# Performance work log

Measured on AMD Instinct MI355X. Metric: run time of the kernel, lower is better.

The kernel has to match this reference:

```python
import jax, jax.numpy as jnp
import numpy as np

N_VERTS = 778
N_JOINTS_CHAIN = 16  # wrist + 15 articulated joints
N_JOINTS_ALL = 21
PARENTS = np.array([0, 0, 1, 2, 0, 4, 5, 0, 7, 8, 0, 10, 11, 0, 13, 14])


def rodrigues(r):
    """Axis-angle [N,3] -> rotation matrices [N,3,3] (matches torch quat2mat path)."""
    angle = jnp.linalg.norm(r + 1e-8, axis=1, keepdims=True)  # [N,1]
    axis = r / angle
    c = jnp.cos(angle)[..., None]  # [N,1,1]
    s = jnp.sin(angle)[..., None]
    x, y, z = axis[:, 0], axis[:, 1], axis[:, 2]
    zero = jnp.zeros_like(x)
    K = jnp.stack([zero, -z, y,
                   z, zero, -x,
                   -y, x, zero], axis=1).reshape(-1, 3, 3)
    eye = jnp.eye(3, dtype=r.dtype)
    return eye + s * K + (1.0 - c) * jnp.matmul(K, K)


def make_A(R, t):
    """R [B,3,3], t [B,3] -> homogeneous [B,4,4]."""
    B = R.shape[0]
    top = jnp.concatenate([R, t[:, :, None]], axis=2)  # [B,3,4]
    bottom = jnp.broadcast_to(jnp.array([[[0., 0., 0., 1.]]], dtype=R.dtype), (B, 1, 4))
    return jnp.concatenate([top, bottom], axis=1)


def setup_inputs() -> dict:
    key = jax.random.key(0)
    ks = jax.random.split(key, 10)
    B = 8192
    w = jax.random.uniform(ks[9], (N_VERTS, 16), dtype=jnp.float32)
    w = w / jnp.sum(w, axis=1, keepdims=True)  # LBS weights rows sum to 1
    Jr = jax.random.uniform(ks[6], (N_VERTS, N_JOINTS_ALL), dtype=jnp.float32)
    Jr = Jr / jnp.sum(Jr, axis=0, keepdims=True)
    return {
        "beta": jax.random.normal(ks[0], (B, 10), dtype=jnp.float32) * 0.5,
        "theta": jax.random.normal(ks[1], (B, 10), dtype=jnp.float32) * 0.5,
        "wrist_euler": jax.random.normal(ks[2], (B, 3), dtype=jnp.float32) * 0.3,
        "v_template": jax.random.normal(ks[3], (N_VERTS, 3), dtype=jnp.float32) * 0.05,
        "shapedirs": jax.random.normal(ks[4], (10, N_VERTS * 3), dtype=jnp.float32) * 0.01,
        "posedirs": jax.random.normal(ks[5], (135, N_VERTS * 3), dtype=jnp.float32) * 0.01,
        "J_regressor": Jr,
        "hands_comp": jax.random.normal(ks[7], (10, 45), dtype=jnp.float32) * 0.5,
        "hands_mean": jax.random.normal(ks[8], (45,), dtype=jnp.float32) * 0.1,
        "weights": w,
    }


def reference(beta, theta, wrist_euler, v_template, shapedirs, posedirs,
              J_regressor, hands_comp, hands_mean, weights):
    B = beta.shape[0]
    # shape blendshapes
    v_shaped = jnp.matmul(beta, shapedirs).reshape(B, N_VERTS, 3) + v_template
    # joints from shaped template: [B,21,3]
    J = jnp.einsum('bvc,vj->bjc', v_shaped, J_regressor)
    # pca pose -> per-joint axis-angle -> rotation matrices
    euler_pose = jnp.matmul(theta, hands_comp) + hands_mean          # [B,45]
    Rs = rodrigues(euler_pose.reshape(-1, 3)).reshape(B, 15, 3, 3)
    global_rot = rodrigues(wrist_euler.reshape(-1, 3)).reshape(B, 1, 3, 3)
    # pose blendshapes: (Rs - I) flattened
    pose_feature = (Rs - jnp.eye(3, dtype=Rs.dtype)).reshape(B, 135)
    v_posed = v_shaped + jnp.matmul(pose_feature, posedirs).reshape(B, N_VERTS, 3)
    # kinematic chain (16 joints, fixed small loop)
    Rs_all = jnp.concatenate([global_rot, Rs], axis=1)  # [B,16,3,3]
    Jc = J[:, :N_JOINTS_CHAIN, :]
    results = [make_A(Rs_all[:, 0], Jc[:, 0])]
    for i in range(1, N_JOINTS_CHAIN):
        p = int(PARENTS[i])
        A_local = make_A(Rs_all[:, i], Jc[:, i] - Jc[:, p])
        results.append(jnp.matmul(results[p], A_local))
    G = jnp.stack(results, axis=1)  # [B,16,4,4]
    # subtract rest-pose joint locations: A = G - G @ [J;0] in last column
    Jh = jnp.concatenate([Jc, jnp.zeros((B, N_JOINTS_CHAIN, 1), Jc.dtype)], axis=2)
    GJ = jnp.einsum('bjpq,bjq->bjp', G, Jh)  # [B,16,4]
    A = G - jnp.concatenate([jnp.zeros((B, N_JOINTS_CHAIN, 4, 3), G.dtype), GJ[..., None]], axis=3)
    # linear blend skinning
    T = jnp.einsum('vj,bjpq->bvpq', weights, A)  # [B,778,4,4]
    v_posed_h = jnp.concatenate([v_posed, jnp.ones((B, N_VERTS, 1), v_posed.dtype)], axis=2)
    verts = jnp.einsum('bvpq,bvq->bvp', T, v_posed_h)[:, :, :3]
    joints = jnp.einsum('bvc,vj->bjc', verts, J_regressor)  # [B,21,3]
    return joints
```

## Files before the change

kernel.cpp:

```cpp
#include <hip/hip_runtime.h>
#include <math.h>

#define NV 778
#define KROW 2334
#define KTOT 146
#define NCOL 1008
#define NPART 16
#define DTLD 160

__global__ __launch_bounds__(64) void kA_pre(const float* __restrict__ shapedirs,
                                             const float* __restrict__ posedirs,
                                             const float* __restrict__ v_template,
                                             const float* __restrict__ Jreg,
                                             const float* __restrict__ wgt,
                                             float* __restrict__ SJ, float* __restrict__ J0,
                                             float* __restrict__ Q,  float* __restrict__ W2,
                                             float* __restrict__ DT, int w2_blocks)
{
    const int bid = blockIdx.x;
    const int t = threadIdx.x;
    if (bid < 48) {
        const int j = bid / 3, c = bid % 3;
        float acc[11];
#pragma unroll
        for (int k = 0; k < 11; ++k) acc[k] = 0.f;
        for (int v = t; v < NV; v += 64) {
            const float jr = Jreg[v*21 + j];
            acc[10] += v_template[v*3 + c] * jr;
#pragma unroll
            for (int k = 0; k < 10; ++k)
                acc[k] += shapedirs[(size_t)k*KROW + v*3 + c] * jr;
        }
#pragma unroll
        for (int k = 0; k < 11; ++k) {
            float s = acc[k];
#pragma unroll
            for (int off = 32; off >= 1; off >>= 1) s += __shfl_down(s, off, 64);
            acc[k] = s;
        }
        if (t == 0) {
#pragma unroll
            for (int k = 0; k < 10; ++k) SJ[k*48 + j*3 + c] = acc[k];
            J0[j*3 + c] = acc[10];
        }
    } else if (bid < 384) {
        const int m = bid - 48, j = m >> 4, jj = m & 15;
        float s = 0.f;
        for (int v = t; v < NV; v += 64)
            s += Jreg[v*21 + j] * wgt[v*16 + jj];
#pragma unroll
        for (int off = 32; off >= 1; off >>= 1) s += __shfl_down(s, off, 64);
        if (t == 0) Q[m] = s;
    } else if (bid < 384 + w2_blocks) {
        const int gi = (bid - 384)*64 + t;
        if (gi < NV*336) {
            const int v = gi / 336, m = gi % 336;
            const int j = m >> 4, jj = m & 15;
            W2[gi] = Jreg[v*21 + j] * wgt[v*16 + jj];
        }
    } else {
        const int v = bid - 384 - w2_blocks;
#pragma unroll
        for (int kk = 0; kk < 3; ++kk) {
            const int k = t + kk*64;
            if (k < KTOT) {
                const float* drow = (k < 10)  ? shapedirs + (size_t)k*KROW
                                  : (k < 145) ? posedirs + (size_t)(k-10)*KROW
                                              : v_template;
                DT[((size_t)0*NV + v)*DTLD + k] = drow[3*v + 0];
                DT[((size_t)1*NV + v)*DTLD + k] = drow[3*v + 1];
                DT[((size_t)2*NV + v)*DTLD + k] = drow[3*v + 2];
            }
        }
    }
}

__global__ __launch_bounds__(192) void k_pre2(const float* __restrict__ DT,
                                              const float* __restrict__ W2,
                                              float* __restrict__ PKpart)
{
    const int bid = blockIdx.x;
    const int j = bid % 21;
    const int c = (bid / 21) % 3;
    const int s = bid / 63;
    const int k = threadIdx.x;
    if (k >= KTOT) return;
    float acc[16];
#pragma unroll
    for (int q = 0; q < 16; ++q) acc[q] = 0.f;
    const int v0 = s*49, v1 = min(NV, v0 + 49);
    const float* dt = DT + ((size_t)c*NV)*DTLD + k;
    for (int v = v0; v < v1; ++v) {
        const float d = dt[(size_t)v*DTLD];
        const float4* wq = (const float4*)(W2 + (size_t)v*336 + j*16);
        const float4 w0 = wq[0], w1 = wq[1], w2 = wq[2], w3 = wq[3];
        acc[0]  += d*w0.x; acc[1]  += d*w0.y; acc[2]  += d*w0.z; acc[3]  += d*w0.w;
        acc[4]  += d*w1.x; acc[5]  += d*w1.y; acc[6]  += d*w1.z; acc[7]  += d*w1.w;
        acc[8]  += d*w2.x; acc[9]  += d*w2.y; acc[10] += d*w2.z; acc[11] += d*w2.w;
        acc[12] += d*w3.x; acc[13] += d*w3.y; acc[14] += d*w3.z; acc[15] += d*w3.w;
    }
    float* o = PKpart + ((size_t)s*KTOT + k)*NCOL + j*48 + c;
#pragma unroll
    for (int q = 0; q < 16; ++q) o[q*3] = acc[q];
}

__global__ void k_p3(const float4* __restrict__ PKpart, float4* __restrict__ PK)
{
    const int n4 = KTOT*NCOL/4;
    const int idx = blockIdx.x*256 + threadIdx.x;
    if (idx < n4) {
        float4 s = PKpart[idx];
#pragma unroll
        for (int p = 1; p < NPART; ++p) {
            const float4 v = PKpart[(size_t)p*n4 + idx];
            s.x += v.x; s.y += v.y; s.z += v.z; s.w += v.w;
        }
        PK[idx] = s;
    }
}

__global__ __launch_bounds__(256) void k2_pose(const float* __restrict__ beta,
                                               const float* __restrict__ theta,
                                               const float* __restrict__ wrist,
                                               const float* __restrict__ hc,
                                               const float* __restrict__ hm,
                                               const float* __restrict__ SJ,
                                               const float* __restrict__ J0,
                                               float* __restrict__ coefT,
                                               float* __restrict__ A_g, int B)
{
    __shared__ float Rs[16*144];
    __shared__ float cls[16*148];
    const int t = threadIdx.x;
    const int bl = t >> 4, i = t & 15;
    const int b = blockIdx.x*16 + bl;

    float r0, r1, r2;
    if (i == 0) {
        r0 = wrist[b*3+0]; r1 = wrist[b*3+1]; r2 = wrist[b*3+2];
#pragma unroll
        for (int k = 0; k < 10; ++k) cls[bl*148 + k] = beta[b*10 + k];
        cls[bl*148 + 145] = 1.0f;
    } else {
        const int col = (i-1)*3;
        float e0 = hm[col], e1 = hm[col+1], e2 = hm[col+2];
#pragma unroll
        for (int k = 0; k < 10; ++k) {
            const float th = theta[b*10 + k];
            e0 += th * hc[k*45 + col];
            e1 += th * hc[k*45 + col+1];
            e2 += th * hc[k*45 + col+2];
        }
        r0 = e0; r1 = e1; r2 = e2;
    }
    const float x_ = r0 + 1e-8f, y_ = r1 + 1e-8f, z_ = r2 + 1e-8f;
    const float angle = sqrtf(x_*x_ + y_*y_ + z_*z_);
    const float inv = 1.0f / angle;
    const float x = r0*inv, y = r1*inv, z = r2*inv;
    const float sn = sinf(angle), cs = cosf(angle);
    const float t1 = 1.0f - cs;
    float R[9];
    R[0] = 1.f - t1*(y*y + z*z);
    R[1] = -sn*z + t1*x*y;
    R[2] =  sn*y + t1*x*z;
    R[3] =  sn*z + t1*x*y;
    R[4] = 1.f - t1*(x*x + z*z);
    R[5] = -sn*x + t1*y*z;
    R[6] = -sn*y + t1*x*z;
    R[7] =  sn*x + t1*y*z;
    R[8] = 1.f - t1*(x*x + y*y);
#pragma unroll
    for (int q = 0; q < 9; ++q) Rs[bl*144 + i*9 + q] = R[q];
    if (i > 0) {
#pragma unroll
        for (int q = 0; q < 9; ++q)
            cls[bl*148 + 10 + (i-1)*9 + q] = R[q] - ((q==0||q==4||q==8) ? 1.f : 0.f);
    }
    __syncthreads();

    if (t < KTOT) {
        float tmp[16];
#pragma unroll
        for (int m = 0; m < 16; ++m) tmp[m] = cls[m*148 + t];
        float4* dst = (float4*)(coefT + (size_t)t*B + blockIdx.x*16);
        dst[0] = make_float4(tmp[0],  tmp[1],  tmp[2],  tmp[3]);
        dst[1] = make_float4(tmp[4],  tmp[5],  tmp[6],  tmp[7]);
        dst[2] = make_float4(tmp[8],  tmp[9],  tmp[10], tmp[11]);
        dst[3] = make_float4(tmp[12], tmp[13], tmp[14], tmp[15]);
    }

    if (t < 16) {
        const int b2 = blockIdx.x*16 + t;
        float bt[10];
#pragma unroll
        for (int k = 0; k < 10; ++k) bt[k] = beta[b2*10 + k];
        const float* Rb = Rs + t*144;
        float4* Ab = (float4*)(A_g + (size_t)b2*192);

        auto jointJ = [&](int j, float* o) {
            float j0 = J0[j*3+0], j1 = J0[j*3+1], j2 = J0[j*3+2];
#pragma unroll
            for (int k = 0; k < 10; ++k) {
                j0 += bt[k] * SJ[k*48 + j*3 + 0];
                j1 += bt[k] * SJ[k*48 + j*3 + 1];
                j2 += bt[k] * SJ[k*48 + j*3 + 2];
            }
            o[0] = j0; o[1] = j1; o[2] = j2;
        };

        float G0R[9], J0v[3];
#pragma unroll
        for (int q = 0; q < 9; ++q) G0R[q] = Rb[q];
        jointJ(0, J0v);
#pragma unroll
        for (int r = 0; r < 3; ++r) {
            const float at = J0v[r] - (G0R[r*3+0]*J0v[0] + G0R[r*3+1]*J0v[1] + G0R[r*3+2]*J0v[2]);
            Ab[r] = make_float4(G0R[r*3+0], G0R[r*3+1], G0R[r*3+2], at);
        }
        for (int ch = 0; ch < 5; ++ch) {
            float GpR[9], Gpt[3], Jp[3];
#pragma unroll
            for (int q = 0; q < 9; ++q) GpR[q] = G0R[q];
            Gpt[0]=J0v[0]; Gpt[1]=J0v[1]; Gpt[2]=J0v[2];
            Jp[0]=J0v[0];  Jp[1]=J0v[1];  Jp[2]=J0v[2];
            for (int s = 0; s < 3; ++s) {
                const int j = ch*3 + 1 + s;
                float Rl[9];
                const float* Rj = Rb + j*9;
#pragma unroll
                for (int q = 0; q < 9; ++q) Rl[q] = Rj[q];
                float Jc[3];
                jointJ(j, Jc);
                const float tl0 = Jc[0]-Jp[0], tl1 = Jc[1]-Jp[1], tl2 = Jc[2]-Jp[2];
                float GR[9], Gt[3];
#pragma unroll
                for (int r = 0; r < 3; ++r) {
#pragma unroll
                    for (int cc = 0; cc < 3; ++cc)
                        GR[r*3+cc] = GpR[r*3+0]*Rl[0*3+cc] + GpR[r*3+1]*Rl[1*3+cc] + GpR[r*3+2]*Rl[2*3+cc];
                    Gt[r] = GpR[r*3+0]*tl0 + GpR[r*3+1]*tl1 + GpR[r*3+2]*tl2 + Gpt[r];
                }
#pragma unroll
                for (int r = 0; r < 3; ++r) {
                    const float at = Gt[r] - (GR[r*3+0]*Jc[0] + GR[r*3+1]*Jc[1] + GR[r*3+2]*Jc[2]);
                    Ab[j*3 + r] = make_float4(GR[r*3+0], GR[r*3+1], GR[r*3+2], at);
                }
#pragma unroll
                for (int q = 0; q < 9; ++q) GpR[q] = GR[q];
                Gpt[0]=Gt[0]; Gpt[1]=Gt[1]; Gpt[2]=Gt[2];
                Jp[0]=Jc[0];  Jp[1]=Jc[1];  Jp[2]=Jc[2];
            }
        }
    }
}

__global__ __launch_bounds__(256) void k3_gemm(const float* __restrict__ coefT,
                                               const float* __restrict__ PK,
                                               const float* __restrict__ A_g,
                                               const float* __restrict__ Q,
                                               float* __restrict__ out, int B)
{
    __shared__ float Pex[48*256];
    const int t  = threadIdx.x;
    const int b0 = blockIdx.x * 256;
    const int j  = blockIdx.y;
    const int ci = __builtin_amdgcn_readfirstlane(t >> 6);
    const int bi = t & 63;

    float acc[12][4];
#pragma unroll
    for (int m = 0; m < 12; ++m)
#pragma unroll
        for (int e = 0; e < 4; ++e) acc[m][e] = 0.f;

    const float* pkbase = PK + j*48 + 4*ci;
    const float* cbase  = coefT + b0 + 4*bi;

#pragma unroll 2
    for (int k = 0; k < KTOT; ++k) {
        const float4 c4 = *(const float4*)(cbase + (size_t)k*B);
        const float* pr = pkbase + (size_t)k*NCOL;
        const float4 p0 = *(const float4*)(pr);
        const float4 p1 = *(const float4*)(pr + 16);
        const float4 p2 = *(const float4*)(pr + 32);
        const float pv[12] = {p0.x,p0.y,p0.z,p0.w, p1.x,p1.y,p1.z,p1.w, p2.x,p2.y,p2.z,p2.w};
        const float cv[4]  = {c4.x,c4.y,c4.z,c4.w};
#pragma unroll
        for (int m = 0; m < 12; ++m)
#pragma unroll
            for (int e = 0; e < 4; ++e)
                acc[m][e] += pv[m] * cv[e];
    }

#pragma unroll
    for (int m = 0; m < 12; ++m) {
        const int col = 16*(m >> 2) + 4*ci + (m & 3);
        *(float4*)(&Pex[col*256 + 4*bi]) =
            make_float4(acc[m][0], acc[m][1], acc[m][2], acc[m][3]);
    }
    __syncthreads();

    {
        const int b = b0 + t;
        const float4* Ab = ((const float4*)A_g) + (size_t)b*48;
        const float* Pr = Pex + t;
        float jx = 0.f, jy = 0.f, jz = 0.f;
#pragma unroll
        for (int jj = 0; jj < 16; ++jj) {
            const float qv = Q[j*16 + jj];
            const float4 a0 = Ab[jj*3+0];
            const float4 a1 = Ab[jj*3+1];
            const float4 a2 = Ab[jj*3+2];
            const float px = Pr[(jj*3+0)*256];
            const float py = Pr[(jj*3+1)*256];
            const float pz = Pr[(jj*3+2)*256];
            jx += a0.x*px + a0.y*py + a0.z*pz + a0.w*qv;
            jy += a1.x*px + a1.y*py + a1.z*pz + a1.w*qv;
            jz += a2.x*px + a2.y*py + a2.z*pz + a2.w*qv;
        }
        float* op = out + (size_t)b*63 + j*3;
        op[0] = jx; op[1] = jy; op[2] = jz;
    }
}

extern "C" void kernel_launch(void* const* d_in, const int* in_sizes, int n_in,
                              void* d_out, int out_size, void* d_ws, size_t ws_size,
                              hipStream_t stream) {
    (void)n_in; (void)out_size; (void)ws_size;
    const float* beta       = (const float*)d_in[0];
    const float* theta      = (const float*)d_in[1];
    const float* wrist      = (const float*)d_in[2];
    const float* v_template = (const float*)d_in[3];
    const float* shapedirs  = (const float*)d_in[4];
    const float* posedirs   = (const float*)d_in[5];
    const float* Jreg       = (const float*)d_in[6];
    const float* hc         = (const float*)d_in[7];
    const float* hm         = (const float*)d_in[8];
    const float* wgt        = (const float*)d_in[9];
    float* out = (float*)d_out;
    const int B = in_sizes[0] / 10;

    float* ws = (float*)d_ws;
    size_t off = 0;
    auto alloc = [&](size_t n) { float* p = ws + off; off = (off + n + 63) & ~(size_t)63; return p; };
    float* SJ     = alloc(480);
    float* J0     = alloc(48);
    float* Q      = alloc(336);
    float* W2     = alloc((size_t)NV*336);
    float* DT     = alloc((size_t)3*NV*DTLD);
    float* PKpart = alloc((size_t)NPART*KTOT*NCOL);
    float* PK     = alloc((size_t)KTOT*NCOL);
    float* coefT  = alloc((size_t)KTOT*B);
    float* A_g    = alloc((size_t)B*192);

    const int w2_blocks = (NV*336 + 63)/64;
    kA_pre<<<384 + w2_blocks + NV, 64, 0, stream>>>(shapedirs, posedirs, v_template,
                                                    Jreg, wgt, SJ, J0, Q, W2, DT, w2_blocks);
    k2_pose<<<(B + 15)/16, 256, 0, stream>>>(beta, theta, wrist, hc, hm, SJ, J0, coefT, A_g, B);
    k_pre2<<<21*3*NPART, 192, 0, stream>>>(DT, W2, PKpart);
    k_p3<<<(KTOT*NCOL/4 + 255)/256, 256, 0, stream>>>((const float4*)PKpart, (float4*)PK);
    k3_gemm<<<dim3(B/256, 21), 256, 0, stream>>>(coefT, PK, A_g, Q, out, B);
}
```

Before: 180.0 us.

## Retile final GEMM so each block covers all joints for 16 batch rows

The final GEMM kernel now uses 512-thread blocks that each handle 16 batch elements across all 21 output joints. Previously each block took 256 batch elements for a single joint on a 2D grid. Each thread accumulates 2 PK columns against 16 coefficients, and the epilogue writes a padded shared-memory tile. The output stores become contiguous. The aim is to reuse A_g and the coefficient loads across joints and to coalesce output writes. In exchange, arithmetic intensity per loaded PK element drops and PK is reread by every block.

```diff
diff --git a/kernel.cpp b/kernel.cpp
--- a/kernel.cpp
+++ b/kernel.cpp
@@ -7,6 +7,7 @@
 #define NCOL 1008
 #define NPART 16
 #define DTLD 160
+#define PEXLD 1032
 
 __global__ __launch_bounds__(64) void kA_pre(const float* __restrict__ shapedirs,
                                              const float* __restrict__ posedirs,
@@ -254,72 +255,67 @@
     }
 }
 
-__global__ __launch_bounds__(256) void k3_gemm(const float* __restrict__ coefT,
+__global__ __launch_bounds__(512) void k3_gemm(const float* __restrict__ coefT,
                                                const float* __restrict__ PK,
                                                const float* __restrict__ A_g,
                                                const float* __restrict__ Q,
                                                float* __restrict__ out, int B)
 {
-    __shared__ float Pex[48*256];
+    __shared__ float Pex[8*PEXLD];
     const int t  = threadIdx.x;
-    const int b0 = blockIdx.x * 256;
-    const int j  = blockIdx.y;
-    const int ci = __builtin_amdgcn_readfirstlane(t >> 6);
-    const int bi = t & 63;
-
-    float acc[12][4];
-#pragma unroll
-    for (int m = 0; m < 12; ++m)
-#pragma unroll
-        for (int e = 0; e < 4; ++e) acc[m][e] = 0.f;
-
-    const float* pkbase = PK + j*48 + 4*ci;
-    const float* cbase  = coefT + b0 + 4*bi;
-
+    const int b0 = blockIdx.x * 16;
+    const int l  = t;
+
+    float acc[2][16];
+#pragma unroll
+    for (int e = 0; e < 16; ++e) { acc[0][e] = 0.f; acc[1][e] = 0.f; }
+
+    if (l < 504) {
+        const float* pkp = PK + 2*l;
+        const float* cof = coefT + b0;
 #pragma unroll 2
-    for (int k = 0; k < KTOT; ++k) {
-        const float4 c4 = *(const float4*)(cbase + (size_t)k*B);
-        const float* pr = pkbase + (size_t)k*NCOL;
-        const float4 p0 = *(const float4*)(pr);
-        const float4 p1 = *(const float4*)(pr + 16);
-        const float4 p2 = *(const float4*)(pr + 32);
-        const float pv[12] = {p0.x,p0.y,p0.z,p0.w, p1.x,p1.y,p1.z,p1.w, p2.x,p2.y,p2.z,p2.w};
-        const float cv[4]  = {c4.x,c4.y,c4.z,c4.w};
-#pragma unroll
-        for (int m = 0; m < 12; ++m)
-#pragma unroll
-            for (int e = 0; e < 4; ++e)
-                acc[m][e] += pv[m] * cv[e];
-    }
-
-#pragma unroll
-    for (int m = 0; m < 12; ++m) {
-        const int col = 16*(m >> 2) + 4*ci + (m & 3);
-        *(float4*)(&Pex[col*256 + 4*bi]) =
-            make_float4(acc[m][0], acc[m][1], acc[m][2], acc[m][3]);
-    }
-    __syncthreads();
-
-    {
-        const int b = b0 + t;
-        const float4* Ab = ((const float4*)A_g) + (size_t)b*48;
-        const float* Pr = Pex + t;
-        float jx = 0.f, jy = 0.f, jz = 0.f;
-#pragma unroll
-        for (int jj = 0; jj < 16; ++jj) {
-            const float qv = Q[j*16 + jj];
-            const float4 a0 = Ab[jj*3+0];
-            const float4 a1 = Ab[jj*3+1];
-            const float4 a2 = Ab[jj*3+2];
-            const float px = Pr[(jj*3+0)*256];
-            const float py = Pr[(jj*3+1)*256];
-            const float pz = Pr[(jj*3+2)*256];
-            jx += a0.x*px + a0.y*py + a0.z*pz + a0.w*qv;
-            jy += a1.x*px + a1.y*py + a1.z*pz + a1.w*qv;
-            jz += a2.x*px + a2.y*py + a2.z*pz + a2.w*qv;
-        }
-        float* op = out + (size_t)b*63 + j*3;
-        op[0] = jx; op[1] = jy; op[2] = jz;
+        for (int k = 0; k < KTOT; ++k) {
+            const float2 p2 = *(const float2*)(pkp + (size_t)k*NCOL);
+            const float4* cp = (const float4*)(cof + (size_t)k*B);
+            const float4 c0 = cp[0], c1 = cp[1], c2 = cp[2], c3 = cp[3];
+            const float cv[16] = {c0.x,c0.y,c0.z,c0.w, c1.x,c1.y,c1.z,c1.w,
+                                  c2.x,c2.y,c2.z,c2.w, c3.x,c3.y,c3.z,c3.w};
+#pragma unroll
+            for (int e = 0; e < 16; ++e) {
+                acc[0][e] += p2.x * cv[e];
+                acc[1][e] += p2.y * cv[e];
+            }
+        }
+    }
+
+#pragma unroll
+    for (int r = 0; r < 2; ++r) {
+        __syncthreads();
+        if (l < 504) {
+            const int j  = (2*l) / 48;
+            const int sc = j*49 + (2*l - 48*j);
+#pragma unroll
+            for (int bb = 0; bb < 8; ++bb)
+                *(float2*)(&Pex[bb*PEXLD + sc]) =
+                    make_float2(acc[0][r*8 + bb], acc[1][r*8 + bb]);
+        }
+        __syncthreads();
+        if (t < 504) {
+            const int bl = t / 63;
+            const int rm = t % 63;
+            const int j  = rm / 3, p = rm % 3;
+            const int b  = b0 + r*8 + bl;
+            const float4* Ab = ((const float4*)A_g) + (size_t)b*48;
+            const float* Pr = Pex + bl*PEXLD + j*49;
+            float s = 0.f;
+#pragma unroll
+            for (int jj = 0; jj < 16; ++jj) {
+                const float4 a = Ab[jj*3 + p];
+                s += a.x*Pr[jj*3+0] + a.y*Pr[jj*3+1] + a.z*Pr[jj*3+2]
+                   + a.w*Q[j*16+jj];
+            }
+            out[(size_t)b0*63 + r*504 + t] = s;
+        }
     }
 }
 
@@ -359,5 +355,5 @@
     k2_pose<<<(B + 15)/16, 256, 0, stream>>>(beta, theta, wrist, hc, hm, SJ, J0, coefT, A_g, B);
     k_pre2<<<21*3*NPART, 192, 0, stream>>>(DT, W2, PKpart);
     k_p3<<<(KTOT*NCOL/4 + 255)/256, 256, 0, stream>>>((const float4*)PKpart, (float4*)PK);
-    k3_gemm<<<dim3(B/256, 21), 256, 0, stream>>>(coefT, PK, A_g, Q, out, B);
-}
+    k3_gemm<<<dim3(B/16), 512, 0, stream>>>(coefT, PK, A_g, Q, out, B);
+}
```

After: 164.2 us. -8.8%, faster.
